# Kernel tuning notes

Hardware: AMD Instinct MI355X
Metric: run time of the kernel (lower is better)

Reference implementation:

```python
import jax, jax.numpy as jnp
import numpy as np
from jax import lax

EPS = 1e-5
IC = 32  # inter_channels

def bn(x, g, b, m, v):
    sh = (1, -1, 1, 1)
    return (x - m.reshape(sh)) * (g.reshape(sh) * lax.rsqrt(v.reshape(sh) + EPS)) + b.reshape(sh)

def prelu(x, a):
    return jnp.where(x >= 0, x, a * x)

def conv1x1(x, w):  # x: [B,C,H,W], w: [O,C]
    return jnp.einsum('bchw,oc->bohw', x, w)

def dconv(x, w, d):  # 3x3 dilated conv, same padding
    return lax.conv_general_dilated(x, w, (1, 1), [(d, d), (d, d)], rhs_dilation=(d, d),
                                    dimension_numbers=('NCHW', 'OIHW', 'NCHW'))

def glca_forward(feature, q_w, q_gamma, q_beta, q_mean, q_var, q_alpha,
                 k_w, k_gamma, k_beta, k_mean, k_var, k_alpha,
                 v_w, v_gamma, v_beta, v_mean, v_var, v_alpha,
                 d1_w, d1_gamma, d1_beta, d1_mean, d1_var,
                 d2_w, d2_gamma, d2_beta, d2_mean, d2_var,
                 d3_w, d3_gamma, d3_beta, d3_mean, d3_var,
                 o_w, o_gamma, o_beta, o_mean, o_var, o_alpha):
    B, C, H, W = feature.shape
    q = prelu(bn(conv1x1(feature, q_w), q_gamma, q_beta, q_mean, q_var), q_alpha)  # [B,IC,H,W]
    k = prelu(bn(conv1x1(feature, k_w), k_gamma, k_beta, k_mean, k_var), k_alpha)
    val = prelu(bn(conv1x1(feature, v_w), v_gamma, v_beta, v_mean, v_var), v_alpha)
    qr = q.transpose(0, 3, 2, 1).reshape(B * W, H, IC)   # [BW,H,IC]
    kr = k.transpose(0, 3, 1, 2).reshape(B * W, IC, H)   # [BW,IC,H]
    att = jax.nn.softmax(jnp.matmul(qr, kr), axis=-1)    # [BW,H,H]
    branches = []
    for w, g, b, m, var, d in ((d1_w, d1_gamma, d1_beta, d1_mean, d1_var, 1),
                               (d2_w, d2_gamma, d2_beta, d2_mean, d2_var, 3),
                               (d3_w, d3_gamma, d3_beta, d3_mean, d3_var, 5)):
        t = jax.nn.relu(bn(dconv(val, w, d), g, b, m, var))          # [B,IC,H,W]
        # faithful to source: permute(0,3,1,2) then raw view to [BW,H,IC]
        t = t.transpose(0, 3, 1, 2).reshape(B * W, H, IC)
        branches.append(jnp.matmul(att, t))                          # [BW,H,IC]
    # faithful to source: cat along dim 0, then raw view(B,W,H,-1)
    res = jnp.concatenate(branches, axis=0).reshape(B, W, H, 3 * IC)
    res = res.transpose(0, 3, 2, 1)                                  # [B,3*IC,H,W]
    out = prelu(bn(conv1x1(res, o_w), o_gamma, o_beta, o_mean, o_var) + feature, o_alpha)
    return out

def setup_inputs() -> dict:
    B, C, H, W = 8, 256, 160, 160
    key = jax.random.key(0)
    ks = iter(jax.random.split(key, 48))
    d = {}
    d['feature'] = jax.random.normal(next(ks), (B, C, H, W), jnp.float32)
    for p in ('q', 'k', 'v'):
        d[p + '_w'] = jax.random.normal(next(ks), (IC, C), jnp.float32) * 0.05
        d[p + '_gamma'] = jax.random.uniform(next(ks), (IC,), jnp.float32, 0.5, 1.5)
        d[p + '_beta'] = jax.random.normal(next(ks), (IC,), jnp.float32) * 0.1
        d[p + '_mean'] = jax.random.normal(next(ks), (IC,), jnp.float32) * 0.1
        d[p + '_var'] = jax.random.uniform(next(ks), (IC,), jnp.float32, 0.5, 1.5)
        d[p + '_alpha'] = jnp.full((1,), 0.25, jnp.float32)
    for p in ('d1', 'd2', 'd3'):
        d[p + '_w'] = jax.random.normal(next(ks), (IC, IC, 3, 3), jnp.float32) * 0.05
        d[p + '_gamma'] = jax.random.uniform(next(ks), (IC,), jnp.float32, 0.5, 1.5)
        d[p + '_beta'] = jax.random.normal(next(ks), (IC,), jnp.float32) * 0.1
        d[p + '_mean'] = jax.random.normal(next(ks), (IC,), jnp.float32) * 0.1
        d[p + '_var'] = jax.random.uniform(next(ks), (IC,), jnp.float32, 0.5, 1.5)
    d['o_w'] = jax.random.normal(next(ks), (C, 3 * IC), jnp.float32) * 0.05
    d['o_gamma'] = jax.random.uniform(next(ks), (C,), jnp.float32, 0.5, 1.5)
    d['o_beta'] = jax.random.normal(next(ks), (C,), jnp.float32) * 0.1
    d['o_mean'] = jax.random.normal(next(ks), (C,), jnp.float32) * 0.1
    d['o_var'] = jax.random.uniform(next(ks), (C,), jnp.float32, 0.5, 1.5)
    d['o_alpha'] = jnp.full((1,), 0.25, jnp.float32)
    return d

def reference(feature, q_w, q_gamma, q_beta, q_mean, q_var, q_alpha,
              k_w, k_gamma, k_beta, k_mean, k_var, k_alpha,
              v_w, v_gamma, v_beta, v_mean, v_var, v_alpha,
              d1_w, d1_gamma, d1_beta, d1_mean, d1_var,
              d2_w, d2_gamma, d2_beta, d2_mean, d2_var,
              d3_w, d3_gamma, d3_beta, d3_mean, d3_var,
              o_w, o_gamma, o_beta, o_mean, o_var, o_alpha):
    return glca_forward(feature, q_w, q_gamma, q_beta, q_mean, q_var, q_alpha,
                        k_w, k_gamma, k_beta, k_mean, k_var, k_alpha,
                        v_w, v_gamma, v_beta, v_mean, v_var, v_alpha,
                        d1_w, d1_gamma, d1_beta, d1_mean, d1_var,
                        d2_w, d2_gamma, d2_beta, d2_mean, d2_var,
                        d3_w, d3_gamma, d3_beta, d3_mean, d3_var,
                        o_w, o_gamma, o_beta, o_mean, o_var, o_alpha)
```

## Files before the change

kernel.cpp:

```cpp
#include <hip/hip_runtime.h>

constexpr int Hh = 160, Ww = 160, Bb = 8, Cc = 256, ICn = 32;
constexpr int HWn = Hh * Ww;
constexpr float EPSf = 1e-5f;

constexpr int P_WQH  = 0;
constexpr int P_WQL  = 12288;
constexpr int P_QKVB = 24576;
constexpr int P_QKVA = 24672;
constexpr int P_DWB  = 24768;
constexpr int P_DB   = 52416;
constexpr int P_OWB  = 52512;
constexpr int P_OB   = 77088;
constexpr int P_OA   = 77344;
constexpr int PLANE  = Bb * ICn * HWn;
constexpr int OFF_Q  = 77824;
constexpr int OFF_K  = OFF_Q + PLANE;
constexpr int OFF_V  = OFF_Q + 2 * PLANE;
constexpr int OFF_T  = OFF_Q + 3 * PLANE;
constexpr int OFF_TPF= OFF_T + (3 * PLANE) / 2;
constexpr int OFF_CAT= OFF_Q + 6 * PLANE;

typedef unsigned short u16;
typedef short bf16x8 __attribute__((ext_vector_type(8)));
typedef float f32x4  __attribute__((ext_vector_type(4)));

__device__ __forceinline__ unsigned f2b(float x) {
    unsigned u = __float_as_uint(x);
    return (u + 0x7FFFu + ((u >> 16) & 1u)) >> 16;
}
__device__ __forceinline__ float b2f(unsigned b) { return __uint_as_float(b << 16); }

struct InPtrs { const float* p[40]; };

__global__ void k_prep(InPtrs in, float* __restrict__ ws) {
    int idx = blockIdx.x * 256 + threadIdx.x;
    if (idx < 24576) {
        int oc = idx >> 8, c = idx & 255;
        int z = oc >> 5, o = oc & 31;
        const float* wz = in.p[1 + 6 * z];
        float s = in.p[2 + 6 * z][o] * rsqrtf(in.p[5 + 6 * z][o] + EPSf);
        float wf = wz[o * 256 + c] * s;
        unsigned hi = f2b(wf);
        unsigned lo = f2b(wf - b2f(hi));
        ((u16*)(ws + P_WQH))[oc * 256 + c] = (u16)hi;
        ((u16*)(ws + P_WQL))[oc * 256 + c] = (u16)lo;
    } else if (idx < 24672) {
        int oc = idx - 24576; int z = oc >> 5, o = oc & 31;
        float s = in.p[2 + 6 * z][o] * rsqrtf(in.p[5 + 6 * z][o] + EPSf);
        ws[P_QKVB + oc] = in.p[3 + 6 * z][o] - in.p[4 + 6 * z][o] * s;
    } else if (idx < 24768) {
        int oc = idx - 24672; int z = oc >> 5;
        ws[P_QKVA + oc] = in.p[6 + 6 * z][0];
    } else if (idx < 52416) {
        int j = idx - 24768;
        int d = j / 9216, r2 = j % 9216;
        int oc = r2 & 31; int tmp = r2 >> 5;
        int kx = tmp % 3; tmp /= 3; int ky = tmp % 3; int ic2 = tmp / 3;
        const float* wd = in.p[19 + 5 * d];
        float s = in.p[20 + 5 * d][oc] * rsqrtf(in.p[23 + 5 * d][oc] + EPSf);
        float wf = wd[((oc * 32 + ic2) * 3 + ky) * 3 + kx] * s;
        ((u16*)(ws + P_DWB))[((d * 9 + ky * 3 + kx) * 32 + oc) * 32 + ic2] = (u16)f2b(wf);
    } else if (idx < 52512) {
        int j = idx - 52416; int d = j >> 5, oc = j & 31;
        float s = in.p[20 + 5 * d][oc] * rsqrtf(in.p[23 + 5 * d][oc] + EPSf);
        ws[P_DB + j] = in.p[21 + 5 * d][oc] - in.p[22 + 5 * d][oc] * s;
    } else if (idx < 77088) {
        int j2 = idx - 52512; int c = j2 / 96;
        float s = in.p[35][c] * rsqrtf(in.p[38][c] + EPSf);
        ((u16*)(ws + P_OWB))[j2] = (u16)f2b(in.p[34][j2] * s);
    } else if (idx < 77344) {
        int c = idx - 77088;
        float s = in.p[35][c] * rsqrtf(in.p[38][c] + EPSf);
        ws[P_OB + c] = in.p[36][c] - in.p[37][c] * s;
    } else if (idx == 77344) {
        ws[P_OA] = in.p[39][0];
    }
}

__global__ __launch_bounds__(64) void k_vpad(float* __restrict__ ws) {
    u16* Vt = (u16*)(ws + OFF_V);
    size_t base = (size_t)blockIdx.x * 176 * 32;
    int t = threadIdx.x;
    int off = (t < 32) ? t * 8 : (168 * 32 + (t - 32) * 8);
    uint4 z = {0u, 0u, 0u, 0u};
    *(uint4*)(Vt + base + off) = z;
}

__global__ __launch_bounds__(256) void k_qkv(const float* __restrict__ feat,
                                             float* __restrict__ ws) {
    __shared__ float FS[64 * 132];
    const int tid = threadIdx.x;
    const int wv = tid >> 6, l = tid & 63;
    const int g = l >> 4, c15 = l & 15;
    const int n0 = blockIdx.x * 128;
    const int b = n0 / HWn, hw0 = n0 % HWn;
    const float* fbase = feat + (size_t)b * Cc * HWn + hw0;
    const u16* __restrict__ WQH = (const u16*)(ws + P_WQH);
    const u16* __restrict__ WQL = (const u16*)(ws + P_WQL);

    f32x4 acc[6][2];
    f32x4 z4 = {0.f, 0.f, 0.f, 0.f};
#pragma unroll
    for (int mt = 0; mt < 6; mt++) { acc[mt][0] = z4; acc[mt][1] = z4; }

    for (int kc = 0; kc < 4; kc++) {
        __syncthreads();
#pragma unroll
        for (int i = 0; i < 8; i++) {
            int f = tid + i * 256;
            int row = f >> 5, col4 = f & 31;
            float4 v = *(const float4*)(fbase + (size_t)(kc * 64 + row) * HWn + col4 * 4);
            *(float4*)(&FS[row * 132 + col4 * 4]) = v;
        }
        __syncthreads();
#pragma unroll
        for (int ks = 0; ks < 2; ks++) {
            bf16x8 bh[2], bl[2];
#pragma unroll
            for (int ntl = 0; ntl < 2; ntl++) {
                int pos = (wv * 2 + ntl) * 16 + c15;
                unsigned hw_[4], lw_[4];
#pragma unroll
                for (int v2 = 0; v2 < 4; v2++) {
                    float x0 = FS[(ks * 32 + g * 8 + 2 * v2) * 132 + pos];
                    float x1 = FS[(ks * 32 + g * 8 + 2 * v2 + 1) * 132 + pos];
                    unsigned h0 = f2b(x0), h1 = f2b(x1);
                    unsigned l0 = f2b(x0 - b2f(h0)), l1 = f2b(x1 - b2f(h1));
                    hw_[v2] = h0 | (h1 << 16);
                    lw_[v2] = l0 | (l1 << 16);
                }
                uint4 hv = {hw_[0], hw_[1], hw_[2], hw_[3]};
                uint4 lv = {lw_[0], lw_[1], lw_[2], lw_[3]};
                bh[ntl] = *(bf16x8*)&hv;
                bl[ntl] = *(bf16x8*)&lv;
            }
#pragma unroll
            for (int mt = 0; mt < 6; mt++) {
                int arow = (16 * mt + c15) * 256 + kc * 64 + ks * 32 + g * 8;
                bf16x8 ah = *(const bf16x8*)(WQH + arow);
                bf16x8 al = *(const bf16x8*)(WQL + arow);
#pragma unroll
                for (int ntl = 0; ntl < 2; ntl++) {
                    acc[mt][ntl] = __builtin_amdgcn_mfma_f32_16x16x32_bf16(ah, bh[ntl], acc[mt][ntl], 0, 0, 0);
                    acc[mt][ntl] = __builtin_amdgcn_mfma_f32_16x16x32_bf16(ah, bl[ntl], acc[mt][ntl], 0, 0, 0);
                    acc[mt][ntl] = __builtin_amdgcn_mfma_f32_16x16x32_bf16(al, bh[ntl], acc[mt][ntl], 0, 0, 0);
                }
            }
        }
    }

    u16* vt = (u16*)(ws + OFF_V);
#pragma unroll
    for (int mt = 0; mt < 6; mt++)
#pragma unroll
        for (int ntl = 0; ntl < 2; ntl++) {
            int pos = hw0 + (wv * 2 + ntl) * 16 + c15;
            if (mt < 4) {
#pragma unroll
                for (int jr = 0; jr < 4; jr++) {
                    int oc = 16 * mt + 4 * g + jr;
                    float bb = ws[P_QKVB + oc];
                    float aa = ws[P_QKVA + oc];
                    float y = acc[mt][ntl][jr] + bb;
                    y = y >= 0.f ? y : aa * y;
                    int z = oc >> 5, o = oc & 31;
                    ws[OFF_Q + (size_t)z * PLANE + ((size_t)b * ICn + o) * HWn + pos] = y;
                }
            } else {
                int h = pos / 160, w2 = pos % 160;
                unsigned r[2];
#pragma unroll
                for (int p = 0; p < 2; p++) {
                    int oc = 16 * mt + 4 * g + 2 * p;
                    float y0 = acc[mt][ntl][2 * p]     + ws[P_QKVB + oc];
                    float y1 = acc[mt][ntl][2 * p + 1] + ws[P_QKVB + oc + 1];
                    float a0 = ws[P_QKVA + oc], a1 = ws[P_QKVA + oc + 1];
                    y0 = y0 >= 0.f ? y0 : a0 * y0;
                    y1 = y1 >= 0.f ? y1 : a1 * y1;
                    r[p] = f2b(y0) | (f2b(y1) << 16);
                }
                size_t a = ((size_t)(b * 160 + h) * 176 + w2 + 8) * 32 + (mt - 4) * 16 + 4 * g;
                uint2 dd; dd.x = r[0]; dd.y = r[1];
                *(uint2*)(vt + a) = dd;
            }
        }
}

__global__ __launch_bounds__(256) void k_dconv(float* __restrict__ ws) {
    const int tid = threadIdx.x;
    const int wv = tid >> 6, l = tid & 63;
    const int g = l >> 4, c15 = l & 15;
    const int b = blockIdx.y;
    const int d = blockIdx.z;
    const int dil = 1 + 2 * d;
    const int h0 = blockIdx.x * 2;
    const u16* __restrict__ WB = (const u16*)(ws + P_DWB) + d * 9 * 32 * 32;
    bf16x8 wb[9][2];
#pragma unroll
    for (int tap = 0; tap < 9; tap++)
#pragma unroll
        for (int n = 0; n < 2; n++)
            wb[tap][n] = *(const bf16x8*)(WB + ((size_t)tap * 32 + n * 16 + c15) * 32 + g * 8);
    const u16* __restrict__ Vt = (const u16*)(ws + OFF_V) + (size_t)b * 160 * 176 * 32;
    const float bias0 = ws[P_DB + d * 32 + c15];
    const float bias1 = ws[P_DB + d * 32 + 16 + c15];
    u16* __restrict__ tp = (u16*)(ws + OFF_TPF) + (size_t)(d * Bb + b) * ICn * HWn;
    f32x4 z4 = {0.f, 0.f, 0.f, 0.f};

    for (int t5 = 0; t5 < 5; t5++) {
        int t = wv * 5 + t5;
        int h = h0 + (t >= 10);
        int w0 = (t % 10) * 16;
        f32x4 acc0 = z4, acc1 = z4;
#pragma unroll
        for (int ky = 0; ky < 3; ky++) {
            int hh = h + dil * (ky - 1);
            if ((unsigned)hh >= 160u) continue;
            const u16* row = Vt + (size_t)hh * 176 * 32;
#pragma unroll
            for (int kx = 0; kx < 3; kx++) {
                int wbase = w0 + dil * (kx - 1) + 8;
                bf16x8 av = *(const bf16x8*)(row + (size_t)(wbase + c15) * 32 + g * 8);
                acc0 = __builtin_amdgcn_mfma_f32_16x16x32_bf16(av, wb[ky * 3 + kx][0], acc0, 0, 0, 0);
                acc1 = __builtin_amdgcn_mfma_f32_16x16x32_bf16(av, wb[ky * 3 + kx][1], acc1, 0, 0, 0);
            }
        }
        size_t pixb = (size_t)h * 160 + w0 + 4 * g;
        uint2 o0, o1;
        o0.x = f2b(fmaxf(acc0[0] + bias0, 0.f)) | (f2b(fmaxf(acc0[1] + bias0, 0.f)) << 16);
        o0.y = f2b(fmaxf(acc0[2] + bias0, 0.f)) | (f2b(fmaxf(acc0[3] + bias0, 0.f)) << 16);
        o1.x = f2b(fmaxf(acc1[0] + bias1, 0.f)) | (f2b(fmaxf(acc1[1] + bias1, 0.f)) << 16);
        o1.y = f2b(fmaxf(acc1[2] + bias1, 0.f)) | (f2b(fmaxf(acc1[3] + bias1, 0.f)) << 16);
        *(uint2*)(tp + (size_t)c15 * HWn + pixb) = o0;
        *(uint2*)(tp + (size_t)(16 + c15) * HWn + pixb) = o1;
    }
}

__global__ __launch_bounds__(256) void k_tfrag(float* __restrict__ ws) {
    __shared__ u16 fr[4][5120];
    const int tid = threadIdx.x;
    const int wq = blockIdx.x;
    const int b  = blockIdx.y;
    const int d  = blockIdx.z;
    const int w0 = wq * 4;
    const u16* __restrict__ tp = (const u16*)(ws + OFF_TPF) + (size_t)(d * Bb + b) * ICn * HWn;
    for (int i = tid; i < 5120; i += 256) {
        int ic = i / 160, h = i % 160;
        uint2 v = *(const uint2*)(tp + (size_t)ic * HWn + h * Ww + w0);
        fr[0][i] = (u16)(v.x & 0xFFFFu);
        fr[1][i] = (u16)(v.x >> 16);
        fr[2][i] = (u16)(v.y & 0xFFFFu);
        fr[3][i] = (u16)(v.y >> 16);
    }
    __syncthreads();
    u16* __restrict__ tf = (u16*)(ws + OFF_T);
#pragma unroll
    for (int it = 0; it < 10; it++) {
        int W = tid + it * 256;
        int s = W / 640, word = W % 640;
        int slot = word >> 6, lane = word & 63;
        int jc = (lane & 15) | ((slot / 5) << 4);
        int h2b = ((slot % 5) << 5) | (((lane >> 4) & 3) << 3);
        unsigned r[4];
#pragma unroll
        for (int p = 0; p < 4; p++) {
            int f0 = (h2b + 2 * p) * 32 + jc;
            unsigned lo = fr[s][f0];
            unsigned hi = fr[s][f0 + 32];
            r[p] = lo | (hi << 16);
        }
        uint4 o4 = {r[0], r[1], r[2], r[3]};
        *(uint4*)(tf + ((size_t)d * 1280 + b * 160 + w0 + s) * 5120 + word * 8) = o4;
    }
}

__global__ __launch_bounds__(256) void k_qkfrag(float* __restrict__ ws) {
    extern __shared__ float frf[];
    const int tid = threadIdx.x;
    const int wq = blockIdx.x;
    const int b  = blockIdx.y;
    const int z  = blockIdx.z;
    const int w0 = wq * 4;
    const float* __restrict__ in = ws + (z ? OFF_K : OFF_Q) + (size_t)b * ICn * HWn;
    u16* __restrict__ outb = (u16*)(ws + (z ? OFF_TPF : OFF_V));

    for (int i = tid; i < 5120; i += 256) {
        int ic = i / 160, h = i % 160;
        float4 v = *(const float4*)(in + (size_t)ic * HWn + h * 160 + w0);
        frf[0 * 5120 + i] = v.x;
        frf[1 * 5120 + i] = v.y;
        frf[2 * 5120 + i] = v.z;
        frf[3 * 5120 + i] = v.w;
    }
    __syncthreads();
#pragma unroll
    for (int it = 0; it < 10; it++) {
        int W = tid + it * 256;
        int s = W / 640, word = W % 640;
        int lane = word & 63, tau = word >> 6;
        int h = tau * 16 + (lane & 15);
        int icb = (lane >> 4) * 8;
        unsigned hw_[4], lw_[4];
#pragma unroll
        for (int p = 0; p < 4; p++) {
            float x0 = frf[s * 5120 + (icb + 2 * p) * 160 + h];
            float x1 = frf[s * 5120 + (icb + 2 * p + 1) * 160 + h];
            unsigned h0 = f2b(x0), h1 = f2b(x1);
            unsigned l0 = f2b(x0 - b2f(h0)), l1 = f2b(x1 - b2f(h1));
            hw_[p] = h0 | (h1 << 16);
            lw_[p] = l0 | (l1 << 16);
        }
        uint4 hv = {hw_[0], hw_[1], hw_[2], hw_[3]};
        uint4 lv = {lw_[0], lw_[1], lw_[2], lw_[3]};
        size_t o = (size_t)(b * 160 + w0 + s) * 5120 + word * 8;
        *(uint4*)(outb + o) = hv;
        *(uint4*)(outb + (size_t)PLANE + o) = lv;
    }
}

__global__ __launch_bounds__(320) void k_att(float* __restrict__ ws) {
    __shared__ char Sb[51200];
    const int tid = threadIdx.x;
    const int bid = blockIdx.x;
    const int r8 = bid & 7, qq = bid >> 3;
    const int b = qq / 20;
    const int w = r8 * 20 + (qq % 20);
    const int bw = b * Ww + w;
    const int wv = tid >> 6;
    const int l  = tid & 63;
    const int g  = l >> 4;
    const int c  = l & 15;
    const int slice = b * 160 + w;

    const u16* __restrict__ qh = (const u16*)(ws + OFF_V)   + (size_t)slice * 5120;
    const u16* __restrict__ ql = qh + (size_t)PLANE;
    const u16* __restrict__ kh = (const u16*)(ws + OFF_TPF) + (size_t)slice * 5120;
    const u16* __restrict__ kl = kh + (size_t)PLANE;

    bf16x8 bq[2][2];
#pragma unroll
    for (int ct = 0; ct < 2; ct++) {
        int tau = 2 * wv + ct;
        bq[ct][0] = *(const bf16x8*)(qh + (tau * 64 + l) * 8);
        bq[ct][1] = *(const bf16x8*)(ql + (tau * 64 + l) * 8);
    }
    f32x4 acc[10][2];
    f32x4 z4 = {0.f, 0.f, 0.f, 0.f};
#pragma unroll
    for (int rt = 0; rt < 10; rt++) { acc[rt][0] = z4; acc[rt][1] = z4; }
#pragma unroll
    for (int rt = 0; rt < 10; rt++) {
        bf16x8 ah = *(const bf16x8*)(kh + (rt * 64 + l) * 8);
        bf16x8 al = *(const bf16x8*)(kl + (rt * 64 + l) * 8);
#pragma unroll
        for (int ct = 0; ct < 2; ct++) {
            acc[rt][ct] = __builtin_amdgcn_mfma_f32_16x16x32_bf16(ah, bq[ct][0], acc[rt][ct], 0, 0, 0);
            acc[rt][ct] = __builtin_amdgcn_mfma_f32_16x16x32_bf16(ah, bq[ct][1], acc[rt][ct], 0, 0, 0);
            acc[rt][ct] = __builtin_amdgcn_mfma_f32_16x16x32_bf16(al, bq[ct][0], acc[rt][ct], 0, 0, 0);
        }
    }

    float mx[2] = {-3.4e38f, -3.4e38f};
#pragma unroll
    for (int rt = 0; rt < 10; rt++)
#pragma unroll
        for (int ct = 0; ct < 2; ct++)
#pragma unroll
            for (int j = 0; j < 4; j++) mx[ct] = fmaxf(mx[ct], acc[rt][ct][j]);
#pragma unroll
    for (int ct = 0; ct < 2; ct++) {
        mx[ct] = fmaxf(mx[ct], __shfl_xor(mx[ct], 16));
        mx[ct] = fmaxf(mx[ct], __shfl_xor(mx[ct], 32));
    }
    float sm[2] = {0.f, 0.f};
#pragma unroll
    for (int rt = 0; rt < 10; rt++)
#pragma unroll
        for (int ct = 0; ct < 2; ct++)
#pragma unroll
            for (int j = 0; j < 4; j++) {
                float e = __expf(acc[rt][ct][j] - mx[ct]);
                acc[rt][ct][j] = e;
                sm[ct] += e;
            }
#pragma unroll
    for (int ct = 0; ct < 2; ct++) {
        sm[ct] += __shfl_xor(sm[ct], 16);
        sm[ct] += __shfl_xor(sm[ct], 32);
    }
    float inv[2] = {1.f / sm[0], 1.f / sm[1]};

#pragma unroll
    for (int rt = 0; rt < 10; rt++) {
#pragma unroll
        for (int ct = 0; ct < 2; ct++) {
            float p0 = acc[rt][ct][0] * inv[ct];
            float p1 = acc[rt][ct][1] * inv[ct];
            float p2 = acc[rt][ct][2] * inv[ct];
            float p3 = acc[rt][ct][3] * inv[ct];
            unsigned d0 = f2b(p0) | (f2b(p1) << 16);
            unsigned d1 = f2b(p2) | (f2b(p3) << 16);
            int Lf = c + 16 * (2 * (rt & 1) + (g >> 1));
            char* dst = Sb + (((wv * 2 + ct) * 5 + (rt >> 1)) * 64 + Lf) * 16 + 8 * (g & 1);
            uint2 dd; dd.x = d0; dd.y = d1;
            *(uint2*)dst = dd;
        }
    }

    const u16* tf = (const u16*)(ws + OFF_T);
    u16* catb = (u16*)(ws + OFF_CAT);
    for (int d = 0; d < 3; d++) {
        const u16* tfd = tf + ((size_t)d * (Bb * Ww) + bw) * 5120;
        f32x4 po[2][2];
        po[0][0] = z4; po[0][1] = z4; po[1][0] = z4; po[1][1] = z4;
#pragma unroll
        for (int ks = 0; ks < 5; ks++) {
            bf16x8 a0 = *(const bf16x8*)(tfd + ((0 * 5 + ks) * 64 + l) * 8);
            bf16x8 a1 = *(const bf16x8*)(tfd + ((1 * 5 + ks) * 64 + l) * 8);
            bf16x8 s0 = *(bf16x8*)(Sb + (((wv * 2 + 0) * 5 + ks) * 64 + l) * 16);
            bf16x8 s1 = *(bf16x8*)(Sb + (((wv * 2 + 1) * 5 + ks) * 64 + l) * 16);
            po[0][0] = __builtin_amdgcn_mfma_f32_16x16x32_bf16(a0, s0, po[0][0], 0, 0, 0);
            po[0][1] = __builtin_amdgcn_mfma_f32_16x16x32_bf16(a0, s1, po[0][1], 0, 0, 0);
            po[1][0] = __builtin_amdgcn_mfma_f32_16x16x32_bf16(a1, s0, po[1][0], 0, 0, 0);
            po[1][1] = __builtin_amdgcn_mfma_f32_16x16x32_bf16(a1, s1, po[1][1], 0, 0, 0);
        }
#pragma unroll
        for (int jt = 0; jt < 2; jt++)
#pragma unroll
            for (int ct = 0; ct < 2; ct++) {
                int h1 = 32 * wv + 16 * ct + c;
                size_t idx = (size_t)d * PLANE + (size_t)bw * 5120 + h1 * 32 + 16 * jt + 4 * g;
                f32x4 v = po[jt][ct];
                uint2 dd;
                dd.x = f2b(v[0]) | (f2b(v[1]) << 16);
                dd.y = f2b(v[2]) | (f2b(v[3]) << 16);
                *(uint2*)(catb + idx) = dd;
            }
    }
}

__global__ __launch_bounds__(256) void k_out(const float* __restrict__ feat,
                                             const float* __restrict__ ws,
                                             float* __restrict__ out) {
    __shared__ u16 Bs[12288];
    const int tid = threadIdx.x;
    const int wv = tid >> 6, l = tid & 63;
    const int g = l >> 4, c15 = l & 15;
    const int n0 = blockIdx.x * 128;
    const int b = n0 / HWn, hw0 = n0 % HWn;
    const u16* __restrict__ CATb = (const u16*)(ws + OFF_CAT);
    const u16* __restrict__ OWB = (const u16*)(ws + P_OWB);

#pragma unroll
    for (int ss = 0; ss < 6; ss++) {
        int s = tid + ss * 256;
        int sl = s & 63, si = s >> 6;
        int p = (si & 7) * 16 + (sl & 15);
        int hw = hw0 + p;
        int h = hw / Ww, w2 = hw % Ww;
        int j = (si >> 3) * 32 + (sl >> 4) * 8;
        size_t flat = ((size_t)(b * Ww + w2) * Hh + h) * 96 + j;
        *(uint4*)(&Bs[(si * 64 + sl) * 8]) = *(const uint4*)(CATb + flat);
    }
    bf16x8 af[4][3];
#pragma unroll
    for (int mt = 0; mt < 4; mt++)
#pragma unroll
        for (int ks = 0; ks < 3; ks++)
            af[mt][ks] = *(const bf16x8*)(OWB + (wv * 64 + mt * 16 + c15) * 96 + ks * 32 + g * 8);
    __syncthreads();
    const float alpha = ws[P_OA];

    f32x4 z4 = {0.f, 0.f, 0.f, 0.f};
#pragma unroll
    for (int np = 0; np < 2; np++) {
        f32x4 acc[4][4];
#pragma unroll
        for (int mt = 0; mt < 4; mt++)
#pragma unroll
            for (int ntl = 0; ntl < 4; ntl++) acc[mt][ntl] = z4;
#pragma unroll
        for (int ks = 0; ks < 3; ks++) {
            bf16x8 bf_[4];
#pragma unroll
            for (int ntl = 0; ntl < 4; ntl++)
                bf_[ntl] = *(const bf16x8*)(&Bs[((ks * 8 + np * 4 + ntl) * 64 + l) * 8]);
#pragma unroll
            for (int mt = 0; mt < 4; mt++)
#pragma unroll
                for (int ntl = 0; ntl < 4; ntl++)
                    acc[mt][ntl] = __builtin_amdgcn_mfma_f32_16x16x32_bf16(af[mt][ks], bf_[ntl], acc[mt][ntl], 0, 0, 0);
        }
#pragma unroll
        for (int mt = 0; mt < 4; mt++)
#pragma unroll
            for (int ntl = 0; ntl < 4; ntl++) {
                int p = (np * 4 + ntl) * 16 + c15;
#pragma unroll
                for (int jr = 0; jr < 4; jr++) {
                    int cch = wv * 64 + mt * 16 + 4 * g + jr;
                    size_t base = ((size_t)b * Cc + cch) * HWn + hw0 + p;
                    float y = acc[mt][ntl][jr] + ws[P_OB + cch] + feat[base];
                    out[base] = y >= 0.f ? y : alpha * y;
                }
            }
    }
}

extern "C" void kernel_launch(void* const* d_in, const int* in_sizes, int n_in,
                              void* d_out, int out_size, void* d_ws, size_t ws_size,
                              hipStream_t stream) {
    InPtrs ip;
    for (int i = 0; i < 40; i++) ip.p[i] = (const float*)d_in[i];
    float* ws = (float*)d_ws;
    const float* feat = (const float*)d_in[0];
    float* out = (float*)d_out;

    k_prep<<<304, 256, 0, stream>>>(ip, ws);
    k_vpad<<<1280, 64, 0, stream>>>(ws);
    k_qkv<<<1600, 256, 0, stream>>>(feat, ws);
    k_dconv<<<dim3(80, 8, 3), 256, 0, stream>>>(ws);
    k_tfrag<<<dim3(40, 8, 3), 256, 0, stream>>>(ws);
    (void)hipFuncSetAttribute(reinterpret_cast<const void*>(k_qkfrag),
                              hipFuncAttributeMaxDynamicSharedMemorySize, 81920);
    k_qkfrag<<<dim3(40, 8, 2), 256, 81920, stream>>>(ws);
    k_att<<<1280, 320, 0, stream>>>(ws);
    k_out<<<1600, 256, 0, stream>>>(feat, ws, out);
}
```

Measured before the change: 471.2 us.

## Double-buffer feature tiles in QKV projection with register prefetch

Result: faster. 442.6 us, median of 2 (-6.1%).

```diff
diff --git a/kernel.cpp b/kernel.cpp
--- a/kernel.cpp
+++ b/kernel.cpp
@@ -87,9 +87,9 @@
     *(uint4*)(Vt + base + off) = z;
 }
 
-__global__ __launch_bounds__(256) void k_qkv(const float* __restrict__ feat,
-                                             float* __restrict__ ws) {
-    __shared__ float FS[64 * 132];
+__global__ __launch_bounds__(256, 4) void k_qkv(const float* __restrict__ feat,
+                                                float* __restrict__ ws) {
+    __shared__ float FS[2][32 * 132];
     const int tid = threadIdx.x;
     const int wv = tid >> 6, l = tid & 63;
     const int g = l >> 4, c15 = l & 15;
@@ -104,49 +104,70 @@
 #pragma unroll
     for (int mt = 0; mt < 6; mt++) { acc[mt][0] = z4; acc[mt][1] = z4; }
 
-    for (int kc = 0; kc < 4; kc++) {
-        __syncthreads();
-#pragma unroll
-        for (int i = 0; i < 8; i++) {
-            int f = tid + i * 256;
-            int row = f >> 5, col4 = f & 31;
-            float4 v = *(const float4*)(fbase + (size_t)(kc * 64 + row) * HWn + col4 * 4);
-            *(float4*)(&FS[row * 132 + col4 * 4]) = v;
-        }
-        __syncthreads();
-#pragma unroll
-        for (int ks = 0; ks < 2; ks++) {
-            bf16x8 bh[2], bl[2];
+    float4 pre0, pre1, pre2, pre3;
+    {
+        int f0 = tid, f1 = tid + 256, f2 = tid + 512, f3 = tid + 768;
+        pre0 = *(const float4*)(fbase + (size_t)(f0 >> 5) * HWn + (f0 & 31) * 4);
+        pre1 = *(const float4*)(fbase + (size_t)(f1 >> 5) * HWn + (f1 & 31) * 4);
+        pre2 = *(const float4*)(fbase + (size_t)(f2 >> 5) * HWn + (f2 & 31) * 4);
+        pre3 = *(const float4*)(fbase + (size_t)(f3 >> 5) * HWn + (f3 & 31) * 4);
+        *(float4*)(&FS[0][(f0 >> 5) * 132 + (f0 & 31) * 4]) = pre0;
+        *(float4*)(&FS[0][(f1 >> 5) * 132 + (f1 & 31) * 4]) = pre1;
+        *(float4*)(&FS[0][(f2 >> 5) * 132 + (f2 & 31) * 4]) = pre2;
+        *(float4*)(&FS[0][(f3 >> 5) * 132 + (f3 & 31) * 4]) = pre3;
+    }
+    __syncthreads();
+
+    for (int kc = 0; kc < 8; kc++) {
+        const int cur = kc & 1;
+        if (kc < 7) {
+            int base = (kc + 1) * 32;
+            int f0 = tid, f1 = tid + 256, f2 = tid + 512, f3 = tid + 768;
+            pre0 = *(const float4*)(fbase + (size_t)(base + (f0 >> 5)) * HWn + (f0 & 31) * 4);
+            pre1 = *(const float4*)(fbase + (size_t)(base + (f1 >> 5)) * HWn + (f1 & 31) * 4);
+            pre2 = *(const float4*)(fbase + (size_t)(base + (f2 >> 5)) * HWn + (f2 & 31) * 4);
+            pre3 = *(const float4*)(fbase + (size_t)(base + (f3 >> 5)) * HWn + (f3 & 31) * 4);
+        }
+        bf16x8 bh[2], bl[2];
+#pragma unroll
+        for (int ntl = 0; ntl < 2; ntl++) {
+            int pos = (wv * 2 + ntl) * 16 + c15;
+            unsigned hw_[4], lw_[4];
+#pragma unroll
+            for (int v2 = 0; v2 < 4; v2++) {
+                float x0 = FS[cur][(g * 8 + 2 * v2) * 132 + pos];
+                float x1 = FS[cur][(g * 8 + 2 * v2 + 1) * 132 + pos];
+                unsigned h0 = f2b(x0), h1 = f2b(x1);
+                unsigned l0 = f2b(x0 - b2f(h0)), l1 = f2b(x1 - b2f(h1));
+                hw_[v2] = h0 | (h1 << 16);
+                lw_[v2] = l0 | (l1 << 16);
+            }
+            uint4 hv = {hw_[0], hw_[1], hw_[2], hw_[3]};
+            uint4 lv = {lw_[0], lw_[1], lw_[2], lw_[3]};
+            bh[ntl] = *(bf16x8*)&hv;
+            bl[ntl] = *(bf16x8*)&lv;
+        }
+#pragma unroll
+        for (int mt = 0; mt < 6; mt++) {
+            int arow = (16 * mt + c15) * 256 + kc * 32 + g * 8;
+            bf16x8 ah = *(const bf16x8*)(WQH + arow);
+            bf16x8 al = *(const bf16x8*)(WQL + arow);
 #pragma unroll
             for (int ntl = 0; ntl < 2; ntl++) {
-                int pos = (wv * 2 + ntl) * 16 + c15;
-                unsigned hw_[4], lw_[4];
-#pragma unroll
-                for (int v2 = 0; v2 < 4; v2++) {
-                    float x0 = FS[(ks * 32 + g * 8 + 2 * v2) * 132 + pos];
-                    float x1 = FS[(ks * 32 + g * 8 + 2 * v2 + 1) * 132 + pos];
-                    unsigned h0 = f2b(x0), h1 = f2b(x1);
-                    unsigned l0 = f2b(x0 - b2f(h0)), l1 = f2b(x1 - b2f(h1));
-                    hw_[v2] = h0 | (h1 << 16);
-                    lw_[v2] = l0 | (l1 << 16);
-                }
-                uint4 hv = {hw_[0], hw_[1], hw_[2], hw_[3]};
-                uint4 lv = {lw_[0], lw_[1], lw_[2], lw_[3]};
-                bh[ntl] = *(bf16x8*)&hv;
-                bl[ntl] = *(bf16x8*)&lv;
-            }
-#pragma unroll
-            for (int mt = 0; mt < 6; mt++) {
-                int arow = (16 * mt + c15) * 256 + kc * 64 + ks * 32 + g * 8;
-                bf16x8 ah = *(const bf16x8*)(WQH + arow);
-                bf16x8 al = *(const bf16x8*)(WQL + arow);
-#pragma unroll
-                for (int ntl = 0; ntl < 2; ntl++) {
-                    acc[mt][ntl] = __builtin_amdgcn_mfma_f32_16x16x32_bf16(ah, bh[ntl], acc[mt][ntl], 0, 0, 0);
-                    acc[mt][ntl] = __builtin_amdgcn_mfma_f32_16x16x32_bf16(ah, bl[ntl], acc[mt][ntl], 0, 0, 0);
-                    acc[mt][ntl] = __builtin_amdgcn_mfma_f32_16x16x32_bf16(al, bh[ntl], acc[mt][ntl], 0, 0, 0);
-                }
-            }
+                acc[mt][ntl] = __builtin_amdgcn_mfma_f32_16x16x32_bf16(ah, bh[ntl], acc[mt][ntl], 0, 0, 0);
+                acc[mt][ntl] = __builtin_amdgcn_mfma_f32_16x16x32_bf16(ah, bl[ntl], acc[mt][ntl], 0, 0, 0);
+                acc[mt][ntl] = __builtin_amdgcn_mfma_f32_16x16x32_bf16(al, bh[ntl], acc[mt][ntl], 0, 0, 0);
+            }
+        }
+        if (kc < 7) {
+            __syncthreads();
+            int f0 = tid, f1 = tid + 256, f2 = tid + 512, f3 = tid + 768;
+            float* nb = FS[cur ^ 1];
+            *(float4*)(&nb[(f0 >> 5) * 132 + (f0 & 31) * 4]) = pre0;
+            *(float4*)(&nb[(f1 >> 5) * 132 + (f1 & 31) * 4]) = pre1;
+            *(float4*)(&nb[(f2 >> 5) * 132 + (f2 & 31) * 4]) = pre2;
+            *(float4*)(&nb[(f3 >> 5) * 132 + (f3 & 31) * 4]) = pre3;
+            __syncthreads();
         }
     }
 
```

## Software-pipeline QKV feature loads with register prefetch and double-buffered LDS

Applied to the files above, without the earlier changes.

New measurement: 527.9 us. 12.0% more time.

```diff
diff --git a/kernel.cpp b/kernel.cpp
--- a/kernel.cpp
+++ b/kernel.cpp
@@ -87,9 +87,9 @@
     *(uint4*)(Vt + base + off) = z;
 }
 
-__global__ __launch_bounds__(256) void k_qkv(const float* __restrict__ feat,
-                                             float* __restrict__ ws) {
-    __shared__ float FS[64 * 132];
+__global__ __launch_bounds__(256, 3) void k_qkv(const float* __restrict__ feat,
+                                                float* __restrict__ ws) {
+    __shared__ float FS[2][32 * 132];
     const int tid = threadIdx.x;
     const int wv = tid >> 6, l = tid & 63;
     const int g = l >> 4, c15 = l & 15;
@@ -99,54 +99,79 @@
     const u16* __restrict__ WQH = (const u16*)(ws + P_WQH);
     const u16* __restrict__ WQL = (const u16*)(ws + P_WQL);
 
+    const int f0 = tid, f1 = tid + 256, f2 = tid + 512, f3 = tid + 768;
+    const int r0 = f0 >> 5, r1 = f1 >> 5, r2 = f2 >> 5, r3 = f3 >> 5;
+    const int o0 = (f0 & 31) * 4, o1 = (f1 & 31) * 4, o2 = (f2 & 31) * 4, o3 = (f3 & 31) * 4;
+
     f32x4 acc[6][2];
     f32x4 z4 = {0.f, 0.f, 0.f, 0.f};
 #pragma unroll
     for (int mt = 0; mt < 6; mt++) { acc[mt][0] = z4; acc[mt][1] = z4; }
 
-    for (int kc = 0; kc < 4; kc++) {
-        __syncthreads();
-#pragma unroll
-        for (int i = 0; i < 8; i++) {
-            int f = tid + i * 256;
-            int row = f >> 5, col4 = f & 31;
-            float4 v = *(const float4*)(fbase + (size_t)(kc * 64 + row) * HWn + col4 * 4);
-            *(float4*)(&FS[row * 132 + col4 * 4]) = v;
-        }
-        __syncthreads();
-#pragma unroll
-        for (int ks = 0; ks < 2; ks++) {
-            bf16x8 bh[2], bl[2];
+    float4 pre[3][4];
+
+#pragma unroll
+    for (int j = 0; j < 3; j++) {
+        int base = j * 32;
+        pre[j][0] = *(const float4*)(fbase + (size_t)(base + r0) * HWn + o0);
+        pre[j][1] = *(const float4*)(fbase + (size_t)(base + r1) * HWn + o1);
+        pre[j][2] = *(const float4*)(fbase + (size_t)(base + r2) * HWn + o2);
+        pre[j][3] = *(const float4*)(fbase + (size_t)(base + r3) * HWn + o3);
+    }
+    *(float4*)(&FS[0][r0 * 132 + o0]) = pre[0][0];
+    *(float4*)(&FS[0][r1 * 132 + o1]) = pre[0][1];
+    *(float4*)(&FS[0][r2 * 132 + o2]) = pre[0][2];
+    *(float4*)(&FS[0][r3 * 132 + o3]) = pre[0][3];
+    __syncthreads();
+
+#pragma unroll
+    for (int kc = 0; kc < 8; kc++) {
+        bf16x8 bh[2], bl[2];
+#pragma unroll
+        for (int ntl = 0; ntl < 2; ntl++) {
+            int pos = (wv * 2 + ntl) * 16 + c15;
+            unsigned hw_[4], lw_[4];
+#pragma unroll
+            for (int v2 = 0; v2 < 4; v2++) {
+                float x0 = FS[kc & 1][(g * 8 + 2 * v2) * 132 + pos];
+                float x1 = FS[kc & 1][(g * 8 + 2 * v2 + 1) * 132 + pos];
+                unsigned h0 = f2b(x0), h1 = f2b(x1);
+                unsigned l0 = f2b(x0 - b2f(h0)), l1 = f2b(x1 - b2f(h1));
+                hw_[v2] = h0 | (h1 << 16);
+                lw_[v2] = l0 | (l1 << 16);
+            }
+            uint4 hv = {hw_[0], hw_[1], hw_[2], hw_[3]};
+            uint4 lv = {lw_[0], lw_[1], lw_[2], lw_[3]};
+            bh[ntl] = *(bf16x8*)&hv;
+            bl[ntl] = *(bf16x8*)&lv;
+        }
+#pragma unroll
+        for (int mt = 0; mt < 6; mt++) {
+            int arow = (16 * mt + c15) * 256 + kc * 32 + g * 8;
+            bf16x8 ah = *(const bf16x8*)(WQH + arow);
+            bf16x8 al = *(const bf16x8*)(WQL + arow);
 #pragma unroll
             for (int ntl = 0; ntl < 2; ntl++) {
-                int pos = (wv * 2 + ntl) * 16 + c15;
-                unsigned hw_[4], lw_[4];
-#pragma unroll
-                for (int v2 = 0; v2 < 4; v2++) {
-                    float x0 = FS[(ks * 32 + g * 8 + 2 * v2) * 132 + pos];
-                    float x1 = FS[(ks * 32 + g * 8 + 2 * v2 + 1) * 132 + pos];
-                    unsigned h0 = f2b(x0), h1 = f2b(x1);
-                    unsigned l0 = f2b(x0 - b2f(h0)), l1 = f2b(x1 - b2f(h1));
-                    hw_[v2] = h0 | (h1 << 16);
-                    lw_[v2] = l0 | (l1 << 16);
-                }
-                uint4 hv = {hw_[0], hw_[1], hw_[2], hw_[3]};
-                uint4 lv = {lw_[0], lw_[1], lw_[2], lw_[3]};
-                bh[ntl] = *(bf16x8*)&hv;
-                bl[ntl] = *(bf16x8*)&lv;
-            }
-#pragma unroll
-            for (int mt = 0; mt < 6; mt++) {
-                int arow = (16 * mt + c15) * 256 + kc * 64 + ks * 32 + g * 8;
-                bf16x8 ah = *(const bf16x8*)(WQH + arow);
-                bf16x8 al = *(const bf16x8*)(WQL + arow);
-#pragma unroll
-                for (int ntl = 0; ntl < 2; ntl++) {
-                    acc[mt][ntl] = __builtin_amdgcn_mfma_f32_16x16x32_bf16(ah, bh[ntl], acc[mt][ntl], 0, 0, 0);
-                    acc[mt][ntl] = __builtin_amdgcn_mfma_f32_16x16x32_bf16(ah, bl[ntl], acc[mt][ntl], 0, 0, 0);
-                    acc[mt][ntl] = __builtin_amdgcn_mfma_f32_16x16x32_bf16(al, bh[ntl], acc[mt][ntl], 0, 0, 0);
-                }
-            }
+                acc[mt][ntl] = __builtin_amdgcn_mfma_f32_16x16x32_bf16(ah, bh[ntl], acc[mt][ntl], 0, 0, 0);
+                acc[mt][ntl] = __builtin_amdgcn_mfma_f32_16x16x32_bf16(ah, bl[ntl], acc[mt][ntl], 0, 0, 0);
+                acc[mt][ntl] = __builtin_amdgcn_mfma_f32_16x16x32_bf16(al, bh[ntl], acc[mt][ntl], 0, 0, 0);
+            }
+        }
+        if (kc + 3 < 8) {
+            int base = (kc + 3) * 32;
+            pre[kc % 3][0] = *(const float4*)(fbase + (size_t)(base + r0) * HWn + o0);
+            pre[kc % 3][1] = *(const float4*)(fbase + (size_t)(base + r1) * HWn + o1);
+            pre[kc % 3][2] = *(const float4*)(fbase + (size_t)(base + r2) * HWn + o2);
+            pre[kc % 3][3] = *(const float4*)(fbase + (size_t)(base + r3) * HWn + o3);
+        }
+        if (kc < 7) {
+            __syncthreads();
+            float* nb = FS[(kc + 1) & 1];
+            *(float4*)(&nb[r0 * 132 + o0]) = pre[(kc + 1) % 3][0];
+            *(float4*)(&nb[r1 * 132 + o1]) = pre[(kc + 1) % 3][1];
+            *(float4*)(&nb[r2 * 132 + o2]) = pre[(kc + 1) % 3][2];
+            *(float4*)(&nb[r3 * 132 + o3]) = pre[(kc + 1) % 3][3];
+            __syncthreads();
         }
     }
 
```

## Double-buffer feature tiles in QKV projection with register prefetch

Applied to the files above, without the earlier changes.

Result: slower. 490.3 us (+4.1%).

```diff
diff --git a/kernel.cpp b/kernel.cpp
--- a/kernel.cpp
+++ b/kernel.cpp
@@ -87,9 +87,9 @@
     *(uint4*)(Vt + base + off) = z;
 }
 
-__global__ __launch_bounds__(256) void k_qkv(const float* __restrict__ feat,
-                                             float* __restrict__ ws) {
-    __shared__ float FS[64 * 132];
+__global__ __launch_bounds__(256, 4) void k_qkv(const float* __restrict__ feat,
+                                                float* __restrict__ ws) {
+    __shared__ float FS[2][32 * 132];
     const int tid = threadIdx.x;
     const int wv = tid >> 6, l = tid & 63;
     const int g = l >> 4, c15 = l & 15;
@@ -99,56 +99,99 @@
     const u16* __restrict__ WQH = (const u16*)(ws + P_WQH);
     const u16* __restrict__ WQL = (const u16*)(ws + P_WQL);
 
+    const int r0 = tid >> 5, r1 = (tid + 256) >> 5, r2 = (tid + 512) >> 5, r3 = (tid + 768) >> 5;
+    const int o0 = (tid & 31) * 4;
+
     f32x4 acc[6][2];
     f32x4 z4 = {0.f, 0.f, 0.f, 0.f};
 #pragma unroll
     for (int mt = 0; mt < 6; mt++) { acc[mt][0] = z4; acc[mt][1] = z4; }
 
-    for (int kc = 0; kc < 4; kc++) {
+    float4 xA0, xA1, xA2, xA3;
+    float4 xB0, xB1, xB2, xB3;
+
+    xA0 = *(const float4*)(fbase + (size_t)r0 * HWn + o0);
+    xA1 = *(const float4*)(fbase + (size_t)r1 * HWn + o0);
+    xA2 = *(const float4*)(fbase + (size_t)r2 * HWn + o0);
+    xA3 = *(const float4*)(fbase + (size_t)r3 * HWn + o0);
+    xB0 = *(const float4*)(fbase + (size_t)(32 + r0) * HWn + o0);
+    xB1 = *(const float4*)(fbase + (size_t)(32 + r1) * HWn + o0);
+    xB2 = *(const float4*)(fbase + (size_t)(32 + r2) * HWn + o0);
+    xB3 = *(const float4*)(fbase + (size_t)(32 + r3) * HWn + o0);
+    *(float4*)(&FS[0][r0 * 132 + o0]) = xA0;
+    *(float4*)(&FS[0][r1 * 132 + o0]) = xA1;
+    *(float4*)(&FS[0][r2 * 132 + o0]) = xA2;
+    *(float4*)(&FS[0][r3 * 132 + o0]) = xA3;
+    __syncthreads();
+
+#define QKV_COMPUTE(KC, BUF)                                                              \
+    {                                                                                     \
+        bf16x8 bh[2], bl[2];                                                              \
+        _Pragma("unroll")                                                                 \
+        for (int ntl = 0; ntl < 2; ntl++) {                                               \
+            int pos = (wv * 2 + ntl) * 16 + c15;                                          \
+            unsigned hw_[4], lw_[4];                                                      \
+            _Pragma("unroll")                                                             \
+            for (int v2 = 0; v2 < 4; v2++) {                                              \
+                float x0 = FS[BUF][(g * 8 + 2 * v2) * 132 + pos];                         \
+                float x1 = FS[BUF][(g * 8 + 2 * v2 + 1) * 132 + pos];                     \
+                unsigned h0 = f2b(x0), h1 = f2b(x1);                                      \
+                unsigned l0 = f2b(x0 - b2f(h0)), l1 = f2b(x1 - b2f(h1));                  \
+                hw_[v2] = h0 | (h1 << 16);                                                \
+                lw_[v2] = l0 | (l1 << 16);                                                \
+            }                                                                             \
+            uint4 hv = {hw_[0], hw_[1], hw_[2], hw_[3]};                                  \
+            uint4 lv = {lw_[0], lw_[1], lw_[2], lw_[3]};                                  \
+            bh[ntl] = *(bf16x8*)&hv;                                                      \
+            bl[ntl] = *(bf16x8*)&lv;                                                      \
+        }                                                                                 \
+        _Pragma("unroll")                                                                 \
+        for (int mt = 0; mt < 6; mt++) {                                                  \
+            int arow = (16 * mt + c15) * 256 + (KC) * 32 + g * 8;                         \
+            bf16x8 ah = *(const bf16x8*)(WQH + arow);                                     \
+            bf16x8 al = *(const bf16x8*)(WQL + arow);                                     \
+            _Pragma("unroll")                                                             \
+            for (int ntl = 0; ntl < 2; ntl++) {                                           \
+                acc[mt][ntl] = __builtin_amdgcn_mfma_f32_16x16x32_bf16(ah, bh[ntl], acc[mt][ntl], 0, 0, 0); \
+                acc[mt][ntl] = __builtin_amdgcn_mfma_f32_16x16x32_bf16(ah, bl[ntl], acc[mt][ntl], 0, 0, 0); \
+                acc[mt][ntl] = __builtin_amdgcn_mfma_f32_16x16x32_bf16(al, bh[ntl], acc[mt][ntl], 0, 0, 0); \
+            }                                                                             \
+        }                                                                                 \
+    }
+
+    for (int kc2 = 0; kc2 < 8; kc2 += 2) {
+        if (kc2 + 2 < 8) {
+            int base = (kc2 + 2) * 32;
+            xA0 = *(const float4*)(fbase + (size_t)(base + r0) * HWn + o0);
+            xA1 = *(const float4*)(fbase + (size_t)(base + r1) * HWn + o0);
+            xA2 = *(const float4*)(fbase + (size_t)(base + r2) * HWn + o0);
+            xA3 = *(const float4*)(fbase + (size_t)(base + r3) * HWn + o0);
+        }
+        QKV_COMPUTE(kc2, 0);
         __syncthreads();
-#pragma unroll
-        for (int i = 0; i < 8; i++) {
-            int f = tid + i * 256;
-            int row = f >> 5, col4 = f & 31;
-            float4 v = *(const float4*)(fbase + (size_t)(kc * 64 + row) * HWn + col4 * 4);
-            *(float4*)(&FS[row * 132 + col4 * 4]) = v;
-        }
+        *(float4*)(&FS[1][r0 * 132 + o0]) = xB0;
+        *(float4*)(&FS[1][r1 * 132 + o0]) = xB1;
+        *(float4*)(&FS[1][r2 * 132 + o0]) = xB2;
+        *(float4*)(&FS[1][r3 * 132 + o0]) = xB3;
         __syncthreads();
-#pragma unroll
-        for (int ks = 0; ks < 2; ks++) {
-            bf16x8 bh[2], bl[2];
-#pragma unroll
-            for (int ntl = 0; ntl < 2; ntl++) {
-                int pos = (wv * 2 + ntl) * 16 + c15;
-                unsigned hw_[4], lw_[4];
-#pragma unroll
-                for (int v2 = 0; v2 < 4; v2++) {
-                    float x0 = FS[(ks * 32 + g * 8 + 2 * v2) * 132 + pos];
-                    float x1 = FS[(ks * 32 + g * 8 + 2 * v2 + 1) * 132 + pos];
-                    unsigned h0 = f2b(x0), h1 = f2b(x1);
-                    unsigned l0 = f2b(x0 - b2f(h0)), l1 = f2b(x1 - b2f(h1));
-                    hw_[v2] = h0 | (h1 << 16);
-                    lw_[v2] = l0 | (l1 << 16);
-                }
-                uint4 hv = {hw_[0], hw_[1], hw_[2], hw_[3]};
-                uint4 lv = {lw_[0], lw_[1], lw_[2], lw_[3]};
-                bh[ntl] = *(bf16x8*)&hv;
-                bl[ntl] = *(bf16x8*)&lv;
-            }
-#pragma unroll
-            for (int mt = 0; mt < 6; mt++) {
-                int arow = (16 * mt + c15) * 256 + kc * 64 + ks * 32 + g * 8;
-                bf16x8 ah = *(const bf16x8*)(WQH + arow);
-                bf16x8 al = *(const bf16x8*)(WQL + arow);
-#pragma unroll
-                for (int ntl = 0; ntl < 2; ntl++) {
-                    acc[mt][ntl] = __builtin_amdgcn_mfma_f32_16x16x32_bf16(ah, bh[ntl], acc[mt][ntl], 0, 0, 0);
-                    acc[mt][ntl] = __builtin_amdgcn_mfma_f32_16x16x32_bf16(ah, bl[ntl], acc[mt][ntl], 0, 0, 0);
-                    acc[mt][ntl] = __builtin_amdgcn_mfma_f32_16x16x32_bf16(al, bh[ntl], acc[mt][ntl], 0, 0, 0);
-                }
-            }
-        }
-    }
+        if (kc2 + 3 < 8) {
+            int base = (kc2 + 3) * 32;
+            xB0 = *(const float4*)(fbase + (size_t)(base + r0) * HWn + o0);
+            xB1 = *(const float4*)(fbase + (size_t)(base + r1) * HWn + o0);
+            xB2 = *(const float4*)(fbase + (size_t)(base + r2) * HWn + o0);
+            xB3 = *(const float4*)(fbase + (size_t)(base + r3) * HWn + o0);
+        }
+        QKV_COMPUTE(kc2 + 1, 1);
+        if (kc2 + 2 < 8) {
+            __syncthreads();
+            *(float4*)(&FS[0][r0 * 132 + o0]) = xA0;
+            *(float4*)(&FS[0][r1 * 132 + o0]) = xA1;
+            *(float4*)(&FS[0][r2 * 132 + o0]) = xA2;
+            *(float4*)(&FS[0][r3 * 132 + o0]) = xA3;
+            __syncthreads();
+        }
+    }
+#undef QKV_COMPUTE
 
     u16* vt = (u16*)(ws + OFF_V);
 #pragma unroll
```
